# Kernel optimization log

Hardware: AMD Instinct MI355X
Metric: run time of the kernel (lower is better)

Reference implementation:

```python
import jax, jax.numpy as jnp
import numpy as np

N_NODES = 50000
DIM_IN, DIM_H, DIM_OUT = 128, 128, 64


def gcn_conv(x, src, dst, W, b):
    """PyG GCNConv: D^{-1/2}(A+I)D^{-1/2} X W + b, self-loops handled analytically."""
    N = x.shape[0]
    h = x @ W  # [N, dout]
    # in-degree on dst plus 1 for the self loop (PyG computes deg on col/dst)
    deg = jnp.zeros((N,), dtype=x.dtype).at[dst].add(1.0) + 1.0
    dinv = jax.lax.rsqrt(deg)  # deg >= 1 thanks to self loop
    norm = dinv[src] * dinv[dst]  # [E]
    agg = jax.ops.segment_sum(h[src] * norm[:, None], dst, num_segments=N)
    agg = agg + h * (dinv * dinv)[:, None]  # self-loop term: dinv_i^2 * h_i
    return agg + b


def setup_inputs() -> dict:
    key = jax.random.key(0)
    k1, k2, k3, k4, k5 = jax.random.split(key, 5)
    x = jax.random.normal(k1, (N_NODES, DIM_IN), dtype=jnp.float32)
    edge_index = jax.random.randint(k2, (2, 600000), 0, N_NODES, dtype=jnp.int64)
    # Glorot-ish init for weights, zero bias (as in torch defaults for GCNConv)
    W1 = jax.random.normal(k3, (DIM_IN, DIM_H), dtype=jnp.float32) / np.sqrt(DIM_IN)
    b1 = jnp.zeros((DIM_H,), dtype=jnp.float32)
    W2 = jax.random.normal(k4, (DIM_H, DIM_OUT), dtype=jnp.float32) / np.sqrt(DIM_H)
    b2 = jnp.zeros((DIM_OUT,), dtype=jnp.float32)
    return {"x": x, "edge_index": edge_index, "W1": W1, "b1": b1, "W2": W2, "b2": b2}


def reference(x, edge_index, W1, b1, W2, b2):
    src, dst = edge_index[0], edge_index[1]
    h = gcn_conv(x, src, dst, W1, b1)
    h = jax.nn.relu(h)
    h = gcn_conv(h, src, dst, W2, b2)
    return jax.nn.log_softmax(h, axis=1)
```

## Files before the change

### kernel.cpp

```cpp
#include <hip/hip_runtime.h>


typedef short bf16x8 __attribute__((ext_vector_type(8)));
typedef float f32x4 __attribute__((ext_vector_type(4)));
typedef unsigned u32x4 __attribute__((ext_vector_type(4)));

static constexpr int CAP = 64;

static __device__ __forceinline__ short f2bf(float f) {
  union { float f; unsigned u; } v; v.f = f;
  unsigned r = v.u + 0x7fff + ((v.u >> 16) & 1);
  return (short)(r >> 16);
}
static __device__ __forceinline__ float bf2f(unsigned u16) {
  union { unsigned u; float f; } v; v.u = u16 << 16; return v.f;
}
static __device__ __forceinline__ float dinv_of(int cur, int node) {
  return rsqrtf((float)(cur - (node << 6) + 1));
}


__global__ __launch_bounds__(256) void k_init(const float* __restrict__ W1,
                                              const float* __restrict__ W2,
                                              unsigned short* __restrict__ WT1,
                                              unsigned short* __restrict__ WT2,
                                              int* __restrict__ cursor, int n) {
  int t = blockIdx.x * 256 + threadIdx.x;
  if (t < n) cursor[t] = t << 6;
  if (t < 128 * 128) {
    int k = t >> 7, nn = t & 127;
    WT1[nn * 128 + k] = (unsigned short)f2bf(W1[t]);
  }
  if (t < 128 * 64) {
    int k = t >> 6, nn = t & 63;
    WT2[nn * 128 + k] = (unsigned short)f2bf(W2[t]);
  }
}


__global__ __launch_bounds__(256) void k_fill(const int* __restrict__ src,
                                              const int* __restrict__ dst,
                                              int* __restrict__ cursor,
                                              int* __restrict__ col, int E) {
  int e = blockIdx.x * 256 + threadIdx.x;
  if (e < E) {
    int d = dst[e];
    int pos = atomicAdd(&cursor[d], 1);
    if (pos < (d << 6) + CAP) col[pos] = src[e];
  }
}

template <int BN, bool ABF16>
static __device__ __forceinline__ void gemm_body(
    int bid, int tid, const void* __restrict__ Xv,
    const unsigned short* __restrict__ WT, const int* __restrict__ cursor,
    unsigned short* __restrict__ Hout, int n, unsigned char* WL) {
  constexpr int NT = BN / 16;
  constexpr int PITCH = 272;
  {
    const float4* srcw = (const float4*)WT;
#pragma unroll 4
    for (int q = tid; q < BN * 16; q += 256) {
      int r = q >> 4, c = q & 15;
      *(float4*)(&WL[r * PITCH + c * 16]) = srcw[q];
    }
  }
  __syncthreads();

  int wave = tid >> 6, lane = tid & 63;
  int lr = lane & 15, lg = lane >> 4;
  int row = bid * 64 + wave * 16 + lr;
  int arow = (row < n) ? row : (n - 1);

  bf16x8 af[4];
  if (ABF16) {
    const unsigned short* xr = (const unsigned short*)Xv + (size_t)arow * 128 + lg * 8;
#pragma unroll
    for (int t = 0; t < 4; ++t) af[t] = *(const bf16x8*)(xr + t * 32);
  } else {
    const float* xr = (const float*)Xv + (size_t)arow * 128 + lg * 8;
#pragma unroll
    for (int t = 0; t < 4; ++t) {
      float4 lo = *(const float4*)(xr + t * 32);
      float4 hi = *(const float4*)(xr + t * 32 + 4);
      bf16x8 a;
      a[0] = f2bf(lo.x); a[1] = f2bf(lo.y); a[2] = f2bf(lo.z); a[3] = f2bf(lo.w);
      a[4] = f2bf(hi.x); a[5] = f2bf(hi.y); a[6] = f2bf(hi.z); a[7] = f2bf(hi.w);
      af[t] = a;
    }
  }

  f32x4 acc[NT];
#pragma unroll
  for (int j = 0; j < NT; ++j) acc[j] = (f32x4){0.f, 0.f, 0.f, 0.f};

#pragma unroll
  for (int j = 0; j < NT; ++j) {
    const unsigned char* bp = &WL[(size_t)(j * 16 + lr) * PITCH + lg * 16];
#pragma unroll
    for (int t = 0; t < 4; ++t) {
      bf16x8 bfr = *(const bf16x8*)(bp + t * 64);
      acc[j] = __builtin_amdgcn_mfma_f32_16x16x32_bf16(af[t], bfr, acc[j], 0, 0, 0);
    }
  }

  int crow0 = bid * 64 + wave * 16 + lg * 4;
#pragma unroll
  for (int r = 0; r < 4; ++r) {
    int gr = crow0 + r;
    if (gr < n) {
      float sc = dinv_of(cursor[gr], gr);
#pragma unroll
      for (int j = 0; j < NT; ++j)
        Hout[(size_t)gr * BN + j * 16 + lr] = (unsigned short)f2bf(acc[j][r] * sc);
    }
  }
}

__global__ __launch_bounds__(256) void k_gemm1(const float* __restrict__ X,
                                               const unsigned short* __restrict__ WT,
                                               const int* __restrict__ cursor,
                                               unsigned short* __restrict__ Hout, int n) {
  __shared__ unsigned char WL[128 * 272];
  gemm_body<128, false>(blockIdx.x, threadIdx.x, X, WT, cursor, Hout, n, WL);
}

__global__ __launch_bounds__(256) void k_gemm2(const unsigned short* __restrict__ X,
                                               const unsigned short* __restrict__ WT,
                                               const int* __restrict__ cursor,
                                               unsigned short* __restrict__ Hout, int n) {
  __shared__ unsigned char WL[64 * 272];
  gemm_body<64, true>(blockIdx.x, threadIdx.x, X, WT, cursor, Hout, n, WL);
}


__global__ __launch_bounds__(256) void k_gather128(const int* __restrict__ cursor,
                                                   const int* __restrict__ col,
                                                   const unsigned* __restrict__ H1,
                                                   const float* __restrict__ b,
                                                   unsigned* __restrict__ OUT, int n) {
  int tid = threadIdx.x;
  int lane = tid & 63;
  int g = lane >> 4, sub = lane & 15;
  int node = blockIdx.x * 16 + (tid >> 6) * 4 + g;
  if (node >= n) return;
  int e0 = node << 6;
  int cur = cursor[node];
  float di = dinv_of(cur, node);
  int e1 = min(cur, e0 + CAP);
  const u32x4* H4 = (const u32x4*)H1;
  float acc[8];
#pragma unroll
  for (int j = 0; j < 8; ++j) acc[j] = 0.f;
  int e = e0;
  for (; e + 4 <= e1; e += 4) {
    u32x4 v0 = H4[(size_t)col[e] * 16 + sub];
    u32x4 v1 = H4[(size_t)col[e + 1] * 16 + sub];
    u32x4 v2 = H4[(size_t)col[e + 2] * 16 + sub];
    u32x4 v3 = H4[(size_t)col[e + 3] * 16 + sub];
#pragma unroll
    for (int j = 0; j < 4; ++j) {
      acc[2 * j]     += (bf2f(v0[j] & 0xffff) + bf2f(v1[j] & 0xffff)) +
                        (bf2f(v2[j] & 0xffff) + bf2f(v3[j] & 0xffff));
      acc[2 * j + 1] += (bf2f(v0[j] >> 16) + bf2f(v1[j] >> 16)) +
                        (bf2f(v2[j] >> 16) + bf2f(v3[j] >> 16));
    }
  }
  for (; e < e1; ++e) {
    u32x4 v0 = H4[(size_t)col[e] * 16 + sub];
#pragma unroll
    for (int j = 0; j < 4; ++j) {
      acc[2 * j]     += bf2f(v0[j] & 0xffff);
      acc[2 * j + 1] += bf2f(v0[j] >> 16);
    }
  }
  u32x4 vs = H4[(size_t)node * 16 + sub];
  float4 b0 = *(const float4*)(b + 8 * sub);
  float4 b1 = *(const float4*)(b + 8 * sub + 4);
  float bb[8] = {b0.x, b0.y, b0.z, b0.w, b1.x, b1.y, b1.z, b1.w};
  u32x4 o;
#pragma unroll
  for (int j = 0; j < 4; ++j) {
    float vx = fmaxf((acc[2 * j] + bf2f(vs[j] & 0xffff)) * di + bb[2 * j], 0.f);
    float vy = fmaxf((acc[2 * j + 1] + bf2f(vs[j] >> 16)) * di + bb[2 * j + 1], 0.f);
    o[j] = (unsigned)(unsigned short)f2bf(vx) |
           ((unsigned)(unsigned short)f2bf(vy) << 16);
  }
  ((u32x4*)OUT)[(size_t)node * 16 + sub] = o;
}

__global__ __launch_bounds__(256) void k_gather64_lsm(const int* __restrict__ cursor,
                                                      const int* __restrict__ col,
                                                      const unsigned* __restrict__ H2,
                                                      const float* __restrict__ b,
                                                      float* __restrict__ OUT, int n) {
  int tid = threadIdx.x;
  int lane = tid & 63;
  int g = lane >> 3, sub = lane & 7;
  int node = blockIdx.x * 32 + (tid >> 6) * 8 + g;
  if (node >= n) return;
  int e0 = node << 6;
  int cur = cursor[node];
  float di = dinv_of(cur, node);
  int e1 = min(cur, e0 + CAP);
  const u32x4* H4 = (const u32x4*)H2;
  float acc[8];
#pragma unroll
  for (int j = 0; j < 8; ++j) acc[j] = 0.f;
  int e = e0;
  for (; e + 4 <= e1; e += 4) {
    u32x4 v0 = H4[(size_t)col[e] * 8 + sub];
    u32x4 v1 = H4[(size_t)col[e + 1] * 8 + sub];
    u32x4 v2 = H4[(size_t)col[e + 2] * 8 + sub];
    u32x4 v3 = H4[(size_t)col[e + 3] * 8 + sub];
#pragma unroll
    for (int j = 0; j < 4; ++j) {
      acc[2 * j]     += (bf2f(v0[j] & 0xffff) + bf2f(v1[j] & 0xffff)) +
                        (bf2f(v2[j] & 0xffff) + bf2f(v3[j] & 0xffff));
      acc[2 * j + 1] += (bf2f(v0[j] >> 16) + bf2f(v1[j] >> 16)) +
                        (bf2f(v2[j] >> 16) + bf2f(v3[j] >> 16));
    }
  }
  for (; e < e1; ++e) {
    u32x4 v0 = H4[(size_t)col[e] * 8 + sub];
#pragma unroll
    for (int j = 0; j < 4; ++j) {
      acc[2 * j]     += bf2f(v0[j] & 0xffff);
      acc[2 * j + 1] += bf2f(v0[j] >> 16);
    }
  }
  u32x4 vs = H4[(size_t)node * 8 + sub];
  float4 b0 = *(const float4*)(b + 8 * sub);
  float4 b1 = *(const float4*)(b + 8 * sub + 4);
  float bb[8] = {b0.x, b0.y, b0.z, b0.w, b1.x, b1.y, b1.z, b1.w};
  float v[8];
#pragma unroll
  for (int j = 0; j < 4; ++j) {
    v[2 * j]     = (acc[2 * j] + bf2f(vs[j] & 0xffff)) * di + bb[2 * j];
    v[2 * j + 1] = (acc[2 * j + 1] + bf2f(vs[j] >> 16)) * di + bb[2 * j + 1];
  }
  float m = v[0];
#pragma unroll
  for (int j = 1; j < 8; ++j) m = fmaxf(m, v[j]);
#pragma unroll
  for (int off = 1; off < 8; off <<= 1) m = fmaxf(m, __shfl_xor(m, off));
  float s = 0.f;
#pragma unroll
  for (int j = 0; j < 8; ++j) s += expf(v[j] - m);
#pragma unroll
  for (int off = 1; off < 8; off <<= 1) s += __shfl_xor(s, off);
  float ls = logf(s) + m;
  float4 o0 = make_float4(v[0] - ls, v[1] - ls, v[2] - ls, v[3] - ls);
  float4 o1 = make_float4(v[4] - ls, v[5] - ls, v[6] - ls, v[7] - ls);
  float* op = OUT + (size_t)node * 64 + 8 * sub;
  *(float4*)op = o0;
  *(float4*)(op + 4) = o1;
}


extern "C" void kernel_launch(void* const* d_in, const int* in_sizes, int n_in,
                              void* d_out, int out_size, void* d_ws, size_t ws_size,
                              hipStream_t stream) {
  const float* x  = (const float*)d_in[0];
  const int*   ei = (const int*)d_in[1];
  const float* W1 = (const float*)d_in[2];
  const float* b1 = (const float*)d_in[3];
  const float* W2 = (const float*)d_in[4];
  const float* b2 = (const float*)d_in[5];
  float* out = (float*)d_out;

  const int N = in_sizes[0] / 128;
  const int E = in_sizes[1] / 2;
  const int* src = ei;
  const int* dst = ei + E;
  const int NB = (N + 255) / 256;

  int*            cursor = (int*)d_ws;
  unsigned short* WT1    = (unsigned short*)(cursor + N);
  unsigned short* WT2    = WT1 + 128 * 128;
  int*            col    = (int*)(WT2 + 64 * 128);
  unsigned short* bufH1  = (unsigned short*)(col + (size_t)N * CAP);
  unsigned short* bufR   = bufH1 + (size_t)N * 128;
  unsigned short* bufH2  = bufR + (size_t)N * 128;

  k_init<<<NB, 256, 0, stream>>>(W1, W2, WT1, WT2, cursor, N);
  k_fill<<<(E + 255) / 256, 256, 0, stream>>>(src, dst, cursor, col, E);

  const int gemm_grid = (N + 63) / 64;

  k_gemm1<<<gemm_grid, 256, 0, stream>>>(x, WT1, cursor, bufH1, N);
  k_gather128<<<(N + 15) / 16, 256, 0, stream>>>(cursor, col,
                                                 (const unsigned*)bufH1, b1,
                                                 (unsigned*)bufR, N);

  k_gemm2<<<gemm_grid, 256, 0, stream>>>(bufR, WT2, cursor, bufH2, N);
  k_gather64_lsm<<<(N + 31) / 32, 256, 0, stream>>>(cursor, col,
                                                    (const unsigned*)bufH2, b2,
                                                    out, N);
}
```

Baseline: 111.6 us.

## Build CSR via two-pass shared-memory binning and 16-bit column indices

Replaces the per-edge global atomic scatter into the padded adjacency with two passes. The first bins edges by destination block using shared-memory counters and one global reservation per bin. The second places each edge into its node slot with shared-memory atomics and writes the final cursors. Column indices shrink to 16 bits to cut graph-build and gather traffic. This adds an extra kernel and intermediate buffer, and assumes fewer than 65536 nodes and at most 4096 edges per 256-node bin.

```diff
diff --git a/kernel.cpp b/kernel.cpp
--- a/kernel.cpp
+++ b/kernel.cpp
@@ -5,7 +5,8 @@
 typedef float f32x4 __attribute__((ext_vector_type(4)));
 typedef unsigned u32x4 __attribute__((ext_vector_type(4)));
 
-static constexpr int CAP = 64;
+static constexpr int CAP  = 64;
+static constexpr int CAPB = 4096;
 
 static __device__ __forceinline__ short f2bf(float f) {
   union { float f; unsigned u; } v; v.f = f;
@@ -24,9 +25,9 @@
                                               const float* __restrict__ W2,
                                               unsigned short* __restrict__ WT1,
                                               unsigned short* __restrict__ WT2,
-                                              int* __restrict__ cursor, int n) {
+                                              int* __restrict__ gbin) {
   int t = blockIdx.x * 256 + threadIdx.x;
-  if (t < n) cursor[t] = t << 6;
+  if (t < 256) gbin[t] = 0;
   if (t < 128 * 128) {
     int k = t >> 7, nn = t & 127;
     WT1[nn * 128 + k] = (unsigned short)f2bf(W1[t]);
@@ -38,16 +39,55 @@
 }
 
 
-__global__ __launch_bounds__(256) void k_fill(const int* __restrict__ src,
-                                              const int* __restrict__ dst,
-                                              int* __restrict__ cursor,
-                                              int* __restrict__ col, int E) {
-  int e = blockIdx.x * 256 + threadIdx.x;
-  if (e < E) {
-    int d = dst[e];
-    int pos = atomicAdd(&cursor[d], 1);
-    if (pos < (d << 6) + CAP) col[pos] = src[e];
-  }
+__global__ __launch_bounds__(256) void k_bin(const int* __restrict__ src,
+                                             const int* __restrict__ dst,
+                                             int* __restrict__ gbin,
+                                             unsigned* __restrict__ inter,
+                                             int E, int nbins) {
+  __shared__ int lcount[256];
+  __shared__ int lcur[256];
+  int t = threadIdx.x;
+  lcount[t] = 0;
+  __syncthreads();
+  int base = blockIdx.x * 2048;
+  int end = min(base + 2048, E);
+  for (int i = base + t; i < end; i += 256)
+    atomicAdd(&lcount[dst[i] >> 8], 1);
+  __syncthreads();
+  if (t < nbins && lcount[t] > 0) {
+    int r = atomicAdd(&gbin[t], lcount[t]);
+    lcur[t] = t * CAPB + r;
+  }
+  __syncthreads();
+  for (int i = base + t; i < end; i += 256) {
+    int d = dst[i], s = src[i];
+    int bin = d >> 8;
+    int pos = atomicAdd(&lcur[bin], 1);
+    if (pos < (bin + 1) * CAPB)
+      inter[pos] = (unsigned)(d & 255) | ((unsigned)s << 8);
+  }
+}
+
+
+__global__ __launch_bounds__(256) void k_place(const unsigned* __restrict__ inter,
+                                               const int* __restrict__ gbin,
+                                               unsigned short* __restrict__ col,
+                                               int* __restrict__ cursor, int n) {
+  __shared__ int lcur[256];
+  int b = blockIdx.x, t = threadIdx.x;
+  lcur[t] = 0;
+  __syncthreads();
+  int cnt = min(gbin[b], CAPB);
+  const unsigned* seg = inter + (size_t)b * CAPB;
+  for (int i = t; i < cnt; i += 256) {
+    unsigned p = seg[i];
+    int dl = p & 255;
+    int r = atomicAdd(&lcur[dl], 1);
+    if (r < CAP) col[(size_t)(((b << 8) | dl) << 6) + r] = (unsigned short)(p >> 8);
+  }
+  __syncthreads();
+  int node = (b << 8) | t;
+  if (node < n) cursor[node] = (node << 6) + min(lcur[t], CAP);
 }
 
 template <int BN, bool ABF16>
@@ -135,7 +175,7 @@
 
 
 __global__ __launch_bounds__(256) void k_gather128(const int* __restrict__ cursor,
-                                                   const int* __restrict__ col,
+                                                   const unsigned short* __restrict__ col,
                                                    const unsigned* __restrict__ H1,
                                                    const float* __restrict__ b,
                                                    unsigned* __restrict__ OUT, int n) {
@@ -190,7 +230,7 @@
 }
 
 __global__ __launch_bounds__(256) void k_gather64_lsm(const int* __restrict__ cursor,
-                                                      const int* __restrict__ col,
+                                                      const unsigned short* __restrict__ col,
                                                       const unsigned* __restrict__ H2,
                                                       const float* __restrict__ b,
                                                       float* __restrict__ OUT, int n) {
@@ -273,18 +313,21 @@
   const int E = in_sizes[1] / 2;
   const int* src = ei;
   const int* dst = ei + E;
-  const int NB = (N + 255) / 256;
-
-  int*            cursor = (int*)d_ws;
+  const int NBINS = (N + 255) >> 8;
+
+  int*            gbin   = (int*)d_ws;
+  int*            cursor = gbin + 256;
   unsigned short* WT1    = (unsigned short*)(cursor + N);
   unsigned short* WT2    = WT1 + 128 * 128;
-  int*            col    = (int*)(WT2 + 64 * 128);
-  unsigned short* bufH1  = (unsigned short*)(col + (size_t)N * CAP);
+  unsigned*       inter  = (unsigned*)(WT2 + 64 * 128);
+  unsigned short* col    = (unsigned short*)(inter + (size_t)NBINS * CAPB);
+  unsigned short* bufH1  = col + (size_t)N * CAP;
   unsigned short* bufR   = bufH1 + (size_t)N * 128;
   unsigned short* bufH2  = bufR + (size_t)N * 128;
 
-  k_init<<<NB, 256, 0, stream>>>(W1, W2, WT1, WT2, cursor, N);
-  k_fill<<<(E + 255) / 256, 256, 0, stream>>>(src, dst, cursor, col, E);
+  k_init<<<64, 256, 0, stream>>>(W1, W2, WT1, WT2, gbin);
+  k_bin<<<(E + 2047) / 2048, 256, 0, stream>>>(src, dst, gbin, inter, E, NBINS);
+  k_place<<<NBINS, 256, 0, stream>>>(inter, gbin, col, cursor, N);
 
   const int gemm_grid = (N + 63) / 64;
 
```

After: 100.6 us, median of 2. 9.8% less time.
